# Kernel tuning notes

Hardware: AMD Instinct MI355X
Metric: run time of the kernel (lower is better)

Reference implementation:

```python
import jax, jax.numpy as jnp
import numpy as np

N_NODES = 50000
NUM_FEAT = 128
HIDDEN = 128
NUM_OUT = 40
E_REG = 800000
E_EGO = 1600000


def setup_inputs() -> dict:
    key = jax.random.key(0)
    ks = jax.random.split(key, 12)
    def lin(k, fi, fo):
        s = 1.0 / np.sqrt(fi)
        return jax.random.uniform(k, (fi, fo), jnp.float32, -s, s)
    return {
        "x_in": jax.random.normal(ks[0], (N_NODES, NUM_FEAT), jnp.float32),
        "edge_index_in": jax.random.randint(ks[1], (2, E_REG), 0, N_NODES, jnp.int64),
        "ego_edge_index": jax.random.randint(ks[2], (2, E_EGO), 0, N_NODES, jnp.int64),
        "W1": lin(ks[3], NUM_FEAT, NUM_FEAT),
        "b1": jnp.zeros((NUM_FEAT,), jnp.float32),
        "Wg1": lin(ks[4], NUM_FEAT, HIDDEN),
        "bg1": jnp.zeros((HIDDEN,), jnp.float32),
        "W2": lin(ks[5], HIDDEN, HIDDEN),
        "b2": jnp.zeros((HIDDEN,), jnp.float32),
        "Wg2": lin(ks[6], HIDDEN, NUM_OUT),
        "bg2": jnp.zeros((NUM_OUT,), jnp.float32),
    }


def _do_conv(x, ego_ei, n):
    # spmm with all-ones values over the union of all ego edge lists:
    # out[row] = sum_{(row,col) in ego edges} x[col]; then * (1/numNodes)
    out = jax.ops.segment_sum(x[ego_ei[1]], ego_ei[0], num_segments=n)
    return out * (1.0 / n)


def _gin_agg(x, ei, n):
    # PyG GINConv (eps=0): x_i + sum_{(j,i) in E} x_j
    return x + jax.ops.segment_sum(x[ei[0]], ei[1], num_segments=n)


def reference(x_in, edge_index_in, ego_edge_index, W1, b1, Wg1, bg1, W2, b2, Wg2, bg2):
    n = x_in.shape[0]
    # Layer 1: Ego conv + Linear, relu, GIN, relu
    x = _do_conv(x_in, ego_edge_index, n)
    x = x @ W1 + b1
    x = jax.nn.relu(x)
    x = _gin_agg(x, edge_index_in, n) @ Wg1 + bg1
    x = jax.nn.relu(x)
    # Layer 2: Ego conv + Linear, relu, GIN (no final relu)
    x = _do_conv(x, ego_edge_index, n)
    x = x @ W2 + b2
    x = jax.nn.relu(x)
    x = _gin_agg(x, edge_index_in, n) @ Wg2 + bg2
    return jax.nn.log_softmax(x, axis=1)
```

## Files before the change

### kernel.cpp

```cpp
#include <hip/hip_runtime.h>
#include <hip/hip_bf16.h>
#include <math.h>


#define FEAT 128
#define BSH 6
#define CHUNK 8192
#define CAPB 4096

typedef unsigned short ushort_t;
typedef unsigned int uint_t;
typedef __attribute__((ext_vector_type(8))) short short8;
typedef __attribute__((ext_vector_type(4))) float f32x4;

__device__ inline float bflo(uint_t u) { return __uint_as_float(u << 16); }
__device__ inline float bfhi(uint_t u) { return __uint_as_float(u & 0xFFFF0000u); }
__device__ inline ushort_t f2bf(float f) {
    union { float f; uint_t u; } c; c.f = f;
    uint_t u = c.u;
    return (ushort_t)((u + 0x7FFFu + ((u >> 16) & 1u)) >> 16);
}
__device__ inline uint_t pack2(float lo, float hi) {
    return (uint_t)f2bf(lo) | ((uint_t)f2bf(hi) << 16);
}

__global__ __launch_bounds__(256) void cast_k(
    const float* __restrict__ in, ushort_t* __restrict__ out, int n4)
{
    int i = blockIdx.x * 256 + threadIdx.x;
    if (i >= n4) return;
    float4 v = ((const float4*)in)[i];
    ushort4 o;
    o.x = f2bf(v.x); o.y = f2bf(v.y); o.z = f2bf(v.z); o.w = f2bf(v.w);
    ((ushort4*)out)[i] = o;
}

__global__ __launch_bounds__(256) void wcast_k(
    const float* __restrict__ W, ushort_t* __restrict__ Wt)
{
    int i = blockIdx.x * 256 + threadIdx.x;
    int c = i >> 7, k = i & 127;
    Wt[i] = f2bf(W[k * FEAT + c]);
}

__global__ __launch_bounds__(256) void chunkhist_k(
    const int* __restrict__ dst, int E, uint_t* __restrict__ cnts)
{
    __shared__ uint_t cnt[1024];
    int tid = threadIdx.x;
    int e0 = blockIdx.x * CHUNK;
    int n = min(CHUNK, E - e0);
    for (int b = tid; b < 1024; b += 256) cnt[b] = 0;
    __syncthreads();
    for (int i = tid; i < n; i += 256)
        atomicAdd(&cnt[dst[e0 + i] >> BSH], 1u);
    __syncthreads();
    uint_t* o = cnts + (size_t)blockIdx.x * 1024;
    for (int b = tid; b < 1024; b += 256) o[b] = cnt[b];
}

__global__ __launch_bounds__(1024) void chunkscan_k(
    const uint_t* __restrict__ cnts, int nch,
    int* __restrict__ bstart, uint_t* __restrict__ base)
{
    __shared__ uint_t s[1024];
    int b = threadIdx.x;
    uint_t tot = 0;
    for (int c = 0; c < nch; ++c) tot += cnts[(size_t)c * 1024 + b];
    s[b] = tot; __syncthreads();
    for (int d = 1; d < 1024; d <<= 1) {
        uint_t v = (b >= d) ? s[b - d] : 0;
        __syncthreads();
        s[b] += v;
        __syncthreads();
    }
    uint_t excl = s[b] - tot;
    bstart[b] = (int)excl;
    if (b == 1023) bstart[1024] = (int)s[1023];
    uint_t run = excl;
    for (int c = 0; c < nch; ++c) {
        base[(size_t)c * 1024 + b] = run;
        run += cnts[(size_t)c * 1024 + b];
    }
}

__global__ __launch_bounds__(256) void binscat_k(
    const int* __restrict__ dst, const int* __restrict__ src, int E,
    const uint_t* __restrict__ basearr, uint_t* __restrict__ staged)
{
    __shared__ uint_t cnt[1024];
    __shared__ uint_t sc[1024];
    __shared__ uint_t gbase[1024];
    __shared__ uint_t part[256];
    __shared__ uint_t srt[CHUNK];

    int tid = threadIdx.x;
    int e0 = blockIdx.x * CHUNK;
    int n = min(CHUNK, E - e0);

    for (int i = tid; i < 1024; i += 256) cnt[i] = 0;
    __syncthreads();

    for (int i = tid; i < n; i += 256)
        atomicAdd(&cnt[dst[e0 + i] >> BSH], 1u);
    __syncthreads();

    uint_t a0 = cnt[4*tid], a1 = cnt[4*tid+1], a2 = cnt[4*tid+2], a3 = cnt[4*tid+3];
    uint_t gs = a0 + a1 + a2 + a3;
    part[tid] = gs; __syncthreads();
    for (int d = 1; d < 256; d <<= 1) {
        uint_t v = (tid >= d) ? part[tid - d] : 0;
        __syncthreads();
        part[tid] += v;
        __syncthreads();
    }
    uint_t b4 = part[tid] - gs;
    sc[4*tid]   = b4;
    sc[4*tid+1] = b4 + a0;
    sc[4*tid+2] = b4 + a0 + a1;
    sc[4*tid+3] = b4 + a0 + a1 + a2;
    __syncthreads();

    const uint_t* gb = basearr + (size_t)blockIdx.x * 1024;
    for (int b = tid; b < 1024; b += 256) gbase[b] = gb[b];
    for (int b = tid; b < 1024; b += 256) cnt[b] = sc[b];
    __syncthreads();

    for (int i = tid; i < n; i += 256) {
        int d = dst[e0 + i];
        int s = src[e0 + i];
        uint_t b = (uint_t)(d >> BSH);
        uint_t p = atomicAdd(&cnt[b], 1u);
        srt[p] = (b << 22) | ((uint_t)s << 6) | (uint_t)(d & 63);
    }
    __syncthreads();

    for (int i = tid; i < n; i += 256) {
        uint_t v = srt[i];
        uint_t b = v >> 22;
        staged[gbase[b] + ((uint_t)i - sc[b])] = v & 0x3FFFFFu;
    }
}

__global__ __launch_bounds__(256) void csrfin_k(
    const uint_t* __restrict__ staged, const int* __restrict__ bstart,
    int* __restrict__ deg, int* __restrict__ start, int* __restrict__ col, int N)
{
    __shared__ int ldeg[64], loff[64], lcur[64];
    __shared__ uint_t buf[CAPB];
    int tid = threadIdx.x;
    int b = blockIdx.x;
    int lo = bstart[b];
    int n = bstart[b + 1] - lo;

    if (tid < 64) ldeg[tid] = 0;
    __syncthreads();
    for (int i = tid; i < n; i += 256)
        atomicAdd(&ldeg[staged[lo + i] & 63], 1);
    __syncthreads();
    if (tid == 0) {
        int r = 0;
        for (int j = 0; j < 64; ++j) { loff[j] = r; r += ldeg[j]; }
    }
    __syncthreads();
    if (tid < 64) {
        int node = (b << BSH) + tid;
        if (node < N) { deg[node] = ldeg[tid]; start[node] = lo + loff[tid]; }
        lcur[tid] = loff[tid];
    }
    __syncthreads();
    for (int i = tid; i < n; i += 256) {
        uint_t v = staged[lo + i];
        int p = atomicAdd(&lcur[v & 63], 1);
        if (p < CAPB) buf[p] = v >> 6;
    }
    __syncthreads();
    for (int i = tid; i < n; i += 256) col[lo + i] = (int)buf[i];
}

template<bool SELF>
__global__ __launch_bounds__(256) void csr_agg_bf_k(
    const ushort_t* __restrict__ x, const int* __restrict__ col,
    const int* __restrict__ start, const int* __restrict__ deg,
    ushort_t* __restrict__ out, int N, float scale)
{
    int w = (blockIdx.x * 256 + threadIdx.x) >> 6;
    if (w >= N) return;
    int lane = threadIdx.x & 63;
    int quarter = lane >> 4;
    int q = lane & 15;

    int s0 = start[w];
    int d  = deg[w];

    float a0=0.f,a1=0.f,a2=0.f,a3=0.f,a4=0.f,a5=0.f,a6=0.f,a7=0.f;
    if (SELF && quarter == 0) {
        uint4 u = ((const uint4*)(x + (size_t)w * FEAT))[q];
        a0 = bflo(u.x); a1 = bfhi(u.x);
        a2 = bflo(u.y); a3 = bfhi(u.y);
        a4 = bflo(u.z); a5 = bfhi(u.z);
        a6 = bflo(u.w); a7 = bfhi(u.w);
    }

    int base = quarter << 4;
    for (int j = 0; j < d; j += 64) {
        int rem = d - j;
        int idx = (lane < rem) ? col[s0 + j + lane] : 0;
        int cnt = min(16, max(rem - base, 0));
#pragma unroll 4
        for (int t = 0; t < cnt; ++t) {
            int s = __shfl(idx, base + t);
            uint4 u = ((const uint4*)(x + (size_t)s * FEAT))[q];
            a0 += bflo(u.x); a1 += bfhi(u.x);
            a2 += bflo(u.y); a3 += bfhi(u.y);
            a4 += bflo(u.z); a5 += bfhi(u.z);
            a6 += bflo(u.w); a7 += bfhi(u.w);
        }
    }
    a0 += __shfl_xor(a0, 16); a0 += __shfl_xor(a0, 32);
    a1 += __shfl_xor(a1, 16); a1 += __shfl_xor(a1, 32);
    a2 += __shfl_xor(a2, 16); a2 += __shfl_xor(a2, 32);
    a3 += __shfl_xor(a3, 16); a3 += __shfl_xor(a3, 32);
    a4 += __shfl_xor(a4, 16); a4 += __shfl_xor(a4, 32);
    a5 += __shfl_xor(a5, 16); a5 += __shfl_xor(a5, 32);
    a6 += __shfl_xor(a6, 16); a6 += __shfl_xor(a6, 32);
    a7 += __shfl_xor(a7, 16); a7 += __shfl_xor(a7, 32);

    if (quarter == 0) {
        uint4 o;
        o.x = pack2(a0 * scale, a1 * scale);
        o.y = pack2(a2 * scale, a3 * scale);
        o.z = pack2(a4 * scale, a5 * scale);
        o.w = pack2(a6 * scale, a7 * scale);
        ((uint4*)(out + (size_t)w * FEAT))[q] = o;
    }
}

__global__ __launch_bounds__(256) void lin128_mfma_k(
    const ushort_t* __restrict__ X, const ushort_t* __restrict__ Wt,
    const float* __restrict__ b, ushort_t* __restrict__ Y, int nRows)
{
    __shared__ ushort_t bounce[64 * FEAT];
    int tid = threadIdx.x;
    int wid = tid >> 6, lane = tid & 63;
    int r0 = blockIdx.x * 64 + wid * 16;
    int la = lane & 15;
    int lb = lane >> 4;

    int arow = r0 + la;
    if (arow >= nRows) arow = 0;
    const ushort_t* xr = X + (size_t)arow * FEAT + lb * 8;
    short8 afrag[4];
#pragma unroll
    for (int s = 0; s < 4; ++s)
        afrag[s] = *(const short8*)(xr + s * 32);

    f32x4 acc[8];
#pragma unroll
    for (int t = 0; t < 8; ++t) acc[t] = (f32x4){0.f, 0.f, 0.f, 0.f};

#pragma unroll
    for (int s = 0; s < 4; ++s) {
#pragma unroll
        for (int t = 0; t < 8; ++t) {
            const ushort_t* wp = Wt + (size_t)(t * 16 + la) * FEAT + s * 32 + lb * 8;
            short8 bfrag = *(const short8*)wp;
            acc[t] = __builtin_amdgcn_mfma_f32_16x16x32_bf16(
                afrag[s], bfrag, acc[t], 0, 0, 0);
        }
    }

    ushort_t* slice = bounce + wid * (16 * FEAT);
#pragma unroll
    for (int t = 0; t < 8; ++t) {
        int colc = t * 16 + la;
        float bias = b[colc];
#pragma unroll
        for (int r = 0; r < 4; ++r) {
            int row = lb * 4 + r;
            float v = fmaxf(acc[t][r] + bias, 0.f);
            slice[row * FEAT + colc] = f2bf(v);
        }
    }
    __syncthreads();
#pragma unroll
    for (int i = 0; i < 4; ++i) {
        int e = i * 512 + lane * 8;
        int row = e >> 7, colc = e & 127;
        uint4 v = *(const uint4*)(slice + e);
        int gr = r0 + row;
        if (gr < nRows) *(uint4*)(Y + (size_t)gr * FEAT + colc) = v;
    }
}

__global__ __launch_bounds__(256) void lin40_bf_k(
    const ushort_t* __restrict__ X, const float* __restrict__ W,
    ushort_t* __restrict__ Y, int nRows)
{
    __shared__ float Wl[FEAT * 40];
    int tid = threadIdx.x;
#pragma unroll
    for (int i = 0; i < 5; ++i)
        ((float4*)Wl)[tid + i * 256] = ((const float4*)W)[tid + i * 256];
    __syncthreads();

    int lane = tid & 63;
    int wv = tid >> 6;
    int row = blockIdx.x * 4 + wv;
    if (row >= nRows) return;

    const ushort_t* xr = X + (size_t)row * FEAT;
    float acc = 0.f;
    if (lane < 40) {
        for (int k = 0; k < FEAT; ++k) {
            float xk = __uint_as_float(((uint_t)xr[k]) << 16);
            acc += xk * Wl[k * 40 + lane];
        }
        Y[(size_t)row * 40 + lane] = f2bf(acc);
    }
}

__global__ __launch_bounds__(256) void agg40_lsm_k(
    const ushort_t* __restrict__ y, const int* __restrict__ col,
    const int* __restrict__ start, const int* __restrict__ deg,
    const float* __restrict__ bias, float* __restrict__ out, int N)
{
    int w = (blockIdx.x * 256 + threadIdx.x) >> 6;
    if (w >= N) return;
    int lane = threadIdx.x & 63;
    int half = lane >> 5;
    int q = lane & 31;

    int s0 = start[w];
    int d  = deg[w];

    float ax = 0.f, ay = 0.f;
    if (half == 0 && q < 20) {
        uint_t u = ((const uint_t*)(y + (size_t)w * 40))[q];
        ax = bflo(u); ay = bfhi(u);
    }

    for (int j = 0; j < d; j += 64) {
        int rem = d - j;
        int idx = (lane < rem) ? col[s0 + j + lane] : 0;
        int cnt = half ? min(32, max(rem - 32, 0)) : min(32, rem);
        for (int t = 0; t < cnt; ++t) {
            int s = __shfl(idx, t + (half << 5));
            if (q < 20) {
                uint_t u = ((const uint_t*)(y + (size_t)s * 40))[q];
                ax += bflo(u); ay += bfhi(u);
            }
        }
    }
    ax += __shfl_xor(ax, 32);
    ay += __shfl_xor(ay, 32);

    if (q < 20) {
        ax += bias[2 * q];
        ay += bias[2 * q + 1];
    }
    float mx = (q < 20) ? fmaxf(ax, ay) : -INFINITY;
#pragma unroll
    for (int off = 1; off <= 32; off <<= 1) mx = fmaxf(mx, __shfl_xor(mx, off));
    float ex = (half == 0 && q < 20) ? (expf(ax - mx) + expf(ay - mx)) : 0.f;
#pragma unroll
    for (int off = 1; off <= 32; off <<= 1) ex += __shfl_xor(ex, off);
    float ls = logf(ex);

    if (half == 0 && q < 20) {
        float2 o = make_float2(ax - mx - ls, ay - mx - ls);
        ((float2*)(out + (size_t)w * 40))[q] = o;
    }
}


extern "C" void kernel_launch(void* const* d_in, const int* in_sizes, int n_in,
                              void* d_out, int out_size, void* d_ws, size_t ws_size,
                              hipStream_t stream) {
    const float* x_in = (const float*)d_in[0];
    const int* ei_reg = (const int*)d_in[1];
    const int* ei_ego = (const int*)d_in[2];
    const float* W1  = (const float*)d_in[3];
    const float* b1  = (const float*)d_in[4];
    const float* Wg1 = (const float*)d_in[5];
    const float* bg1 = (const float*)d_in[6];
    const float* W2  = (const float*)d_in[7];
    const float* b2  = (const float*)d_in[8];
    const float* Wg2 = (const float*)d_in[9];
    const float* bg2 = (const float*)d_in[10];
    float* out = (float*)d_out;

    const int N = in_sizes[0] / FEAT;
    const int E_reg = in_sizes[1] / 2;
    const int E_ego = in_sizes[2] / 2;
    const int NB = (N + 63) >> BSH;
    const int nch_e = (E_ego + CHUNK - 1) / CHUNK;
    const int nch_r = (E_reg + CHUNK - 1) / CHUNK;
    const float inv_n = 1.0f / (float)N;

    ushort_t* Xb  = (ushort_t*)d_ws;
    ushort_t* B0  = Xb + (size_t)N * FEAT;
    ushort_t* B1  = B0 + (size_t)N * FEAT;
    ushort_t* Y40 = B1 + (size_t)N * FEAT;
    ushort_t* Wt1 = Y40 + (size_t)N * 40;
    ushort_t* Wtg1 = Wt1 + FEAT * FEAT;
    ushort_t* Wt2 = Wtg1 + FEAT * FEAT;
    int* colE = (int*)(Wt2 + FEAT * FEAT);
    int* colR = colE + E_ego;
    uint_t* stgE = (uint_t*)(colR + E_reg);
    uint_t* stgR = stgE + E_ego;
    int* degE = (int*)(stgR + E_reg);
    int* stE  = degE + N;
    int* degR = stE + N;
    int* stR  = degR + N;
    int* bstE = stR + N;
    int* bstR = bstE + 1025;
    uint_t* cntsE = (uint_t*)(bstR + 1025);
    uint_t* cntsR = cntsE + (size_t)nch_e * 1024;
    uint_t* baseE = cntsR + (size_t)nch_r * 1024;
    uint_t* baseR = baseE + (size_t)nch_e * 1024;

    const int agg_b  = (N + 3) / 4;
    const int mfma_b = (N + 63) / 64;
    const int cast_b = ((N * FEAT / 4) + 255) / 256;

    cast_k<<<cast_b, 256, 0, stream>>>(x_in, Xb, N * FEAT / 4);
    wcast_k<<<64, 256, 0, stream>>>(W1, Wt1);
    wcast_k<<<64, 256, 0, stream>>>(Wg1, Wtg1);
    wcast_k<<<64, 256, 0, stream>>>(W2, Wt2);
    chunkhist_k<<<nch_e, 256, 0, stream>>>(ei_ego, E_ego, cntsE);
    chunkhist_k<<<nch_r, 256, 0, stream>>>(ei_reg + E_reg, E_reg, cntsR);
    chunkscan_k<<<1, 1024, 0, stream>>>(cntsE, nch_e, bstE, baseE);
    chunkscan_k<<<1, 1024, 0, stream>>>(cntsR, nch_r, bstR, baseR);
    binscat_k<<<nch_e, 256, 0, stream>>>(ei_ego, ei_ego + E_ego, E_ego, baseE, stgE);
    binscat_k<<<nch_r, 256, 0, stream>>>(ei_reg + E_reg, ei_reg, E_reg, baseR, stgR);
    csrfin_k<<<NB, 256, 0, stream>>>(stgE, bstE, degE, stE, colE, N);
    csrfin_k<<<NB, 256, 0, stream>>>(stgR, bstR, degR, stR, colR, N);

    csr_agg_bf_k<false><<<agg_b, 256, 0, stream>>>(Xb, colE, stE, degE, B0, N, inv_n);
    lin128_mfma_k<<<mfma_b, 256, 0, stream>>>(B0, Wt1, b1, B1, N);
    csr_agg_bf_k<true><<<agg_b, 256, 0, stream>>>(B1, colR, stR, degR, B0, N, 1.0f);
    lin128_mfma_k<<<mfma_b, 256, 0, stream>>>(B0, Wtg1, bg1, B1, N);

    csr_agg_bf_k<false><<<agg_b, 256, 0, stream>>>(B1, colE, stE, degE, B0, N, inv_n);
    lin128_mfma_k<<<mfma_b, 256, 0, stream>>>(B0, Wt2, b2, B1, N);
    lin40_bf_k<<<agg_b, 256, 0, stream>>>(B1, Wg2, Y40, N);
    agg40_lsm_k<<<agg_b, 256, 0, stream>>>(Y40, colR, stR, degR, bg2, out, N);
}
```

Baseline: 594.7 us.

## Gather FP8-scaled features in CSR aggregation and use MFMA for final 40-wide linear

The input features and the hidden activations that feed the gather-heavy CSR aggregations are now stored as FP8 (activations pre-scaled by a constant), which halves the bytes read per gathered row. The linear kernel emits an FP8 copy next to its bf16 output, and the aggregations undo the scale. The scalar 40-output linear is replaced by an MFMA kernel with weights padded to 48 columns, and the output buffer is reused. This trades numerical precision for less memory traffic, and accuracy against the tolerance is a risk.

```diff
diff --git a/kernel.cpp b/kernel.cpp
--- a/kernel.cpp
+++ b/kernel.cpp
@@ -7,11 +7,14 @@
 #define BSH 6
 #define CHUNK 8192
 #define CAPB 4096
+#define ENC 4096.0f
 
 typedef unsigned short ushort_t;
 typedef unsigned int uint_t;
+typedef unsigned char uchar_t;
 typedef __attribute__((ext_vector_type(8))) short short8;
 typedef __attribute__((ext_vector_type(4))) float f32x4;
+typedef __attribute__((ext_vector_type(2))) float f32x2;
 
 __device__ inline float bflo(uint_t u) { return __uint_as_float(u << 16); }
 __device__ inline float bfhi(uint_t u) { return __uint_as_float(u & 0xFFFF0000u); }
@@ -23,16 +26,23 @@
 __device__ inline uint_t pack2(float lo, float hi) {
     return (uint_t)f2bf(lo) | ((uint_t)f2bf(hi) << 16);
 }
-
-__global__ __launch_bounds__(256) void cast_k(
-    const float* __restrict__ in, ushort_t* __restrict__ out, int n4)
+__device__ inline uint_t pk4f8(float f0, float f1, float f2, float f3) {
+    int w = __builtin_amdgcn_cvt_pk_fp8_f32(f0, f1, 0, false);
+    w = __builtin_amdgcn_cvt_pk_fp8_f32(f2, f3, w, true);
+    return (uint_t)w;
+}
+
+__global__ __launch_bounds__(256) void cast8_k(
+    const float* __restrict__ in, uchar_t* __restrict__ out, int n8)
 {
     int i = blockIdx.x * 256 + threadIdx.x;
-    if (i >= n4) return;
-    float4 v = ((const float4*)in)[i];
-    ushort4 o;
-    o.x = f2bf(v.x); o.y = f2bf(v.y); o.z = f2bf(v.z); o.w = f2bf(v.w);
-    ((ushort4*)out)[i] = o;
+    if (i >= n8) return;
+    float4 v0 = ((const float4*)in)[2 * i];
+    float4 v1 = ((const float4*)in)[2 * i + 1];
+    uint2 o;
+    o.x = pk4f8(v0.x, v0.y, v0.z, v0.w);
+    o.y = pk4f8(v1.x, v1.y, v1.z, v1.w);
+    ((uint2*)out)[i] = o;
 }
 
 __global__ __launch_bounds__(256) void wcast_k(
@@ -41,6 +51,15 @@
     int i = blockIdx.x * 256 + threadIdx.x;
     int c = i >> 7, k = i & 127;
     Wt[i] = f2bf(W[k * FEAT + c]);
+}
+
+__global__ __launch_bounds__(256) void wcast40_k(
+    const float* __restrict__ W, ushort_t* __restrict__ Wt)
+{
+    int i = blockIdx.x * 256 + threadIdx.x;
+    if (i >= 48 * FEAT) return;
+    int c = i >> 7, k = i & 127;
+    Wt[i] = (c < 40) ? f2bf(W[k * 40 + c]) : (ushort_t)0;
 }
 
 __global__ __launch_bounds__(256) void chunkhist_k(
@@ -179,8 +198,8 @@
 }
 
 template<bool SELF>
-__global__ __launch_bounds__(256) void csr_agg_bf_k(
-    const ushort_t* __restrict__ x, const int* __restrict__ col,
+__global__ __launch_bounds__(256) void csr_agg_f8_k(
+    const uchar_t* __restrict__ x8, const int* __restrict__ col,
     const int* __restrict__ start, const int* __restrict__ deg,
     ushort_t* __restrict__ out, int N, float scale)
 {
@@ -195,11 +214,13 @@
 
     float a0=0.f,a1=0.f,a2=0.f,a3=0.f,a4=0.f,a5=0.f,a6=0.f,a7=0.f;
     if (SELF && quarter == 0) {
-        uint4 u = ((const uint4*)(x + (size_t)w * FEAT))[q];
-        a0 = bflo(u.x); a1 = bfhi(u.x);
-        a2 = bflo(u.y); a3 = bfhi(u.y);
-        a4 = bflo(u.z); a5 = bfhi(u.z);
-        a6 = bflo(u.w); a7 = bfhi(u.w);
+        uint2 u = ((const uint2*)(x8 + (size_t)w * FEAT))[q];
+        f32x2 p0 = __builtin_amdgcn_cvt_pk_f32_fp8(u.x, false);
+        f32x2 p1 = __builtin_amdgcn_cvt_pk_f32_fp8(u.x, true);
+        f32x2 p2 = __builtin_amdgcn_cvt_pk_f32_fp8(u.y, false);
+        f32x2 p3 = __builtin_amdgcn_cvt_pk_f32_fp8(u.y, true);
+        a0 = p0[0]; a1 = p0[1]; a2 = p1[0]; a3 = p1[1];
+        a4 = p2[0]; a5 = p2[1]; a6 = p3[0]; a7 = p3[1];
     }
 
     int base = quarter << 4;
@@ -210,11 +231,13 @@
 #pragma unroll 4
         for (int t = 0; t < cnt; ++t) {
             int s = __shfl(idx, base + t);
-            uint4 u = ((const uint4*)(x + (size_t)s * FEAT))[q];
-            a0 += bflo(u.x); a1 += bfhi(u.x);
-            a2 += bflo(u.y); a3 += bfhi(u.y);
-            a4 += bflo(u.z); a5 += bfhi(u.z);
-            a6 += bflo(u.w); a7 += bfhi(u.w);
+            uint2 u = ((const uint2*)(x8 + (size_t)s * FEAT))[q];
+            f32x2 p0 = __builtin_amdgcn_cvt_pk_f32_fp8(u.x, false);
+            f32x2 p1 = __builtin_amdgcn_cvt_pk_f32_fp8(u.x, true);
+            f32x2 p2 = __builtin_amdgcn_cvt_pk_f32_fp8(u.y, false);
+            f32x2 p3 = __builtin_amdgcn_cvt_pk_f32_fp8(u.y, true);
+            a0 += p0[0]; a1 += p0[1]; a2 += p1[0]; a3 += p1[1];
+            a4 += p2[0]; a5 += p2[1]; a6 += p3[0]; a7 += p3[1];
         }
     }
     a0 += __shfl_xor(a0, 16); a0 += __shfl_xor(a0, 32);
@@ -238,12 +261,14 @@
 
 __global__ __launch_bounds__(256) void lin128_mfma_k(
     const ushort_t* __restrict__ X, const ushort_t* __restrict__ Wt,
-    const float* __restrict__ b, ushort_t* __restrict__ Y, int nRows)
+    const float* __restrict__ b, ushort_t* __restrict__ Y,
+    uchar_t* __restrict__ Y8, float enc, int nRows)
 {
     __shared__ ushort_t bounce[64 * FEAT];
     int tid = threadIdx.x;
     int wid = tid >> 6, lane = tid & 63;
-    int r0 = blockIdx.x * 64 + wid * 16;
+    int rb = blockIdx.x * 64;
+    int r0 = rb + wid * 16;
     int la = lane & 15;
     int lb = lane >> 4;
 
@@ -291,32 +316,78 @@
         int gr = r0 + row;
         if (gr < nRows) *(uint4*)(Y + (size_t)gr * FEAT + colc) = v;
     }
-}
-
-__global__ __launch_bounds__(256) void lin40_bf_k(
-    const ushort_t* __restrict__ X, const float* __restrict__ W,
+    if (Y8) {
+#pragma unroll
+        for (int i = 0; i < 4; ++i) {
+            int j = tid + i * 256;
+            int gr = rb + (j >> 4);
+            uint4 u = *(const uint4*)(bounce + j * 8);
+            float f0 = bflo(u.x) * enc, f1 = bfhi(u.x) * enc;
+            float f2 = bflo(u.y) * enc, f3 = bfhi(u.y) * enc;
+            float f4 = bflo(u.z) * enc, f5 = bfhi(u.z) * enc;
+            float f6 = bflo(u.w) * enc, f7 = bfhi(u.w) * enc;
+            uint2 o;
+            o.x = pk4f8(f0, f1, f2, f3);
+            o.y = pk4f8(f4, f5, f6, f7);
+            if (gr < nRows)
+                *(uint2*)(Y8 + (size_t)gr * FEAT + ((j & 15) * 8)) = o;
+        }
+    }
+}
+
+__global__ __launch_bounds__(256) void lin40_mfma_k(
+    const ushort_t* __restrict__ X, const ushort_t* __restrict__ Wt40,
     ushort_t* __restrict__ Y, int nRows)
 {
-    __shared__ float Wl[FEAT * 40];
+    __shared__ ushort_t bounce[64 * 48];
     int tid = threadIdx.x;
-#pragma unroll
-    for (int i = 0; i < 5; ++i)
-        ((float4*)Wl)[tid + i * 256] = ((const float4*)W)[tid + i * 256];
-    __syncthreads();
-
-    int lane = tid & 63;
-    int wv = tid >> 6;
-    int row = blockIdx.x * 4 + wv;
-    if (row >= nRows) return;
-
-    const ushort_t* xr = X + (size_t)row * FEAT;
-    float acc = 0.f;
-    if (lane < 40) {
-        for (int k = 0; k < FEAT; ++k) {
-            float xk = __uint_as_float(((uint_t)xr[k]) << 16);
-            acc += xk * Wl[k * 40 + lane];
-        }
-        Y[(size_t)row * 40 + lane] = f2bf(acc);
+    int wid = tid >> 6, lane = tid & 63;
+    int r0 = blockIdx.x * 64 + wid * 16;
+    int la = lane & 15;
+    int lb = lane >> 4;
+
+    int arow = r0 + la;
+    if (arow >= nRows) arow = 0;
+    const ushort_t* xr = X + (size_t)arow * FEAT + lb * 8;
+    short8 afrag[4];
+#pragma unroll
+    for (int s = 0; s < 4; ++s)
+        afrag[s] = *(const short8*)(xr + s * 32);
+
+    f32x4 acc[3];
+#pragma unroll
+    for (int t = 0; t < 3; ++t) acc[t] = (f32x4){0.f, 0.f, 0.f, 0.f};
+
+#pragma unroll
+    for (int s = 0; s < 4; ++s) {
+#pragma unroll
+        for (int t = 0; t < 3; ++t) {
+            const ushort_t* wp = Wt40 + (size_t)(t * 16 + la) * FEAT + s * 32 + lb * 8;
+            short8 bfrag = *(const short8*)wp;
+            acc[t] = __builtin_amdgcn_mfma_f32_16x16x32_bf16(
+                afrag[s], bfrag, acc[t], 0, 0, 0);
+        }
+    }
+
+    ushort_t* slice = bounce + wid * (16 * 48);
+#pragma unroll
+    for (int t = 0; t < 3; ++t) {
+        int colc = t * 16 + la;
+#pragma unroll
+        for (int r = 0; r < 4; ++r)
+            slice[(lb * 4 + r) * 48 + colc] = f2bf(acc[t][r]);
+    }
+    __syncthreads();
+#pragma unroll
+    for (int i = 0; i < 2; ++i) {
+        int idx = i * 64 + lane;
+        if (idx < 96) {
+            int row = idx / 6, q4 = idx % 6;
+            int gr = r0 + row;
+            if (gr < nRows)
+                *(uint4*)(Y + (size_t)gr * 48 + q4 * 8) =
+                    *(const uint4*)(slice + row * 48 + q4 * 8);
+        }
     }
 }
 
@@ -336,7 +407,7 @@
 
     float ax = 0.f, ay = 0.f;
     if (half == 0 && q < 20) {
-        uint_t u = ((const uint_t*)(y + (size_t)w * 40))[q];
+        uint_t u = ((const uint_t*)(y + (size_t)w * 48))[q];
         ax = bflo(u); ay = bfhi(u);
     }
 
@@ -347,7 +418,7 @@
         for (int t = 0; t < cnt; ++t) {
             int s = __shfl(idx, t + (half << 5));
             if (q < 20) {
-                uint_t u = ((const uint_t*)(y + (size_t)s * 40))[q];
+                uint_t u = ((const uint_t*)(y + (size_t)s * 48))[q];
                 ax += bflo(u); ay += bfhi(u);
             }
         }
@@ -397,15 +468,18 @@
     const int nch_e = (E_ego + CHUNK - 1) / CHUNK;
     const int nch_r = (E_reg + CHUNK - 1) / CHUNK;
     const float inv_n = 1.0f / (float)N;
-
-    ushort_t* Xb  = (ushort_t*)d_ws;
-    ushort_t* B0  = Xb + (size_t)N * FEAT;
+    const float DEC = 1.0f / ENC;
+
+    uchar_t* Xf8  = (uchar_t*)d_ws;
+    ushort_t* B0  = (ushort_t*)(Xf8 + (size_t)N * FEAT);
     ushort_t* B1  = B0 + (size_t)N * FEAT;
-    ushort_t* Y40 = B1 + (size_t)N * FEAT;
-    ushort_t* Wt1 = Y40 + (size_t)N * 40;
+    uchar_t* B1s8 = (uchar_t*)(B1 + (size_t)N * FEAT);
+    ushort_t* Y40p = B0;
+    ushort_t* Wt1  = (ushort_t*)(B1s8 + (size_t)N * FEAT);
     ushort_t* Wtg1 = Wt1 + FEAT * FEAT;
-    ushort_t* Wt2 = Wtg1 + FEAT * FEAT;
-    int* colE = (int*)(Wt2 + FEAT * FEAT);
+    ushort_t* Wt2  = Wtg1 + FEAT * FEAT;
+    ushort_t* Wt40 = Wt2 + FEAT * FEAT;
+    int* colE = (int*)(Wt40 + 48 * FEAT);
     int* colR = colE + E_ego;
     uint_t* stgE = (uint_t*)(colR + E_reg);
     uint_t* stgR = stgE + E_ego;
@@ -422,12 +496,13 @@
 
     const int agg_b  = (N + 3) / 4;
     const int mfma_b = (N + 63) / 64;
-    const int cast_b = ((N * FEAT / 4) + 255) / 256;
-
-    cast_k<<<cast_b, 256, 0, stream>>>(x_in, Xb, N * FEAT / 4);
+    const int c8_b   = ((N * 16) + 255) / 256;
+
+    cast8_k<<<c8_b, 256, 0, stream>>>(x_in, Xf8, N * 16);
     wcast_k<<<64, 256, 0, stream>>>(W1, Wt1);
     wcast_k<<<64, 256, 0, stream>>>(Wg1, Wtg1);
     wcast_k<<<64, 256, 0, stream>>>(W2, Wt2);
+    wcast40_k<<<24, 256, 0, stream>>>(Wg2, Wt40);
     chunkhist_k<<<nch_e, 256, 0, stream>>>(ei_ego, E_ego, cntsE);
     chunkhist_k<<<nch_r, 256, 0, stream>>>(ei_reg + E_reg, E_reg, cntsR);
     chunkscan_k<<<1, 1024, 0, stream>>>(cntsE, nch_e, bstE, baseE);
@@ -437,13 +512,13 @@
     csrfin_k<<<NB, 256, 0, stream>>>(stgE, bstE, degE, stE, colE, N);
     csrfin_k<<<NB, 256, 0, stream>>>(stgR, bstR, degR, stR, colR, N);
 
-    csr_agg_bf_k<false><<<agg_b, 256, 0, stream>>>(Xb, colE, stE, degE, B0, N, inv_n);
-    lin128_mfma_k<<<mfma_b, 256, 0, stream>>>(B0, Wt1, b1, B1, N);
-    csr_agg_bf_k<true><<<agg_b, 256, 0, stream>>>(B1, colR, stR, degR, B0, N, 1.0f);
-    lin128_mfma_k<<<mfma_b, 256, 0, stream>>>(B0, Wtg1, bg1, B1, N);
-
-    csr_agg_bf_k<false><<<agg_b, 256, 0, stream>>>(B1, colE, stE, degE, B0, N, inv_n);
-    lin128_mfma_k<<<mfma_b, 256, 0, stream>>>(B0, Wt2, b2, B1, N);
-    lin40_bf_k<<<agg_b, 256, 0, stream>>>(B1, Wg2, Y40, N);
-    agg40_lsm_k<<<agg_b, 256, 0, stream>>>(Y40, colR, stR, degR, bg2, out, N);
-}
+    csr_agg_f8_k<false><<<agg_b, 256, 0, stream>>>(Xf8, colE, stE, degE, B0, N, inv_n);
+    lin128_mfma_k<<<mfma_b, 256, 0, stream>>>(B0, Wt1, b1, B1, B1s8, ENC, N);
+    csr_agg_f8_k<true><<<agg_b, 256, 0, stream>>>(B1s8, colR, stR, degR, B0, N, DEC);
+    lin128_mfma_k<<<mfma_b, 256, 0, stream>>>(B0, Wtg1, bg1, B1, B1s8, ENC, N);
+
+    csr_agg_f8_k<false><<<agg_b, 256, 0, stream>>>(B1s8, colE, stE, degE, B0, N, inv_n * DEC);
+    lin128_mfma_k<<<mfma_b, 256, 0, stream>>>(B0, Wt2, b2, B1, (uchar_t*)nullptr, 1.0f, N);
+    lin40_mfma_k<<<mfma_b, 256, 0, stream>>>(B1, Wt40, Y40p, N);
+    agg40_lsm_k<<<agg_b, 256, 0, stream>>>(Y40p, colR, stR, degR, bg2, out, N);
+}
```

After: 560.4 us. 1.06x faster.
